# Optimization experiments

Measured on AMD Instinct MI355X. Metric: run time of the kernel, lower is better.

Reference implementation:

```python
import jax, jax.numpy as jnp
import numpy as np

C = 256
EPS = 1e-5


def dwconv3x3(x, w):
    # x: [B,C,H,W], w: [C,1,3,3] depthwise (groups=C)
    return jax.lax.conv_general_dilated(
        x, w, window_strides=(1, 1), padding=((1, 1), (1, 1)),
        dimension_numbers=('NCHW', 'OIHW', 'NCHW'), feature_group_count=x.shape[1])


def bn(x, gamma, beta, mean, var):
    # inference-mode batchnorm over channel dim of NCHW
    inv = gamma * jax.lax.rsqrt(var + EPS)
    return x * inv[:, None, None] + (beta - mean * inv)[:, None, None]


def setup_inputs() -> dict:
    key = jax.random.key(0)
    ks = jax.random.split(key, 8)
    B, H, W = 32, 64, 64
    inp = {
        'x': jax.random.normal(ks[0], (B, C, H, W), jnp.float32),
        'edge_w': jax.random.normal(ks[1], (C, 1, 3, 3), jnp.float32) * 0.1,
        'edge_gamma': jnp.ones((C,), jnp.float32),
        'edge_beta': jnp.zeros((C,), jnp.float32),
        'edge_mean': jnp.zeros((C,), jnp.float32),
        'edge_var': jnp.ones((C,), jnp.float32),
        'fc1_w': jax.random.normal(ks[2], (C // 16, C), jnp.float32) * 0.05,
        'fc2_w': jax.random.normal(ks[3], (C, C // 16), jnp.float32) * 0.05,
        'fusion_w': jax.random.normal(ks[4], (C, 2 * C), jnp.float32) * 0.05,
        'fusion_b': jnp.zeros((C,), jnp.float32),
        'bn1_gamma': jnp.ones((C,), jnp.float32),
        'bn1_beta': jnp.zeros((C,), jnp.float32),
        'bn1_mean': jnp.zeros((C,), jnp.float32),
        'bn1_var': jnp.ones((C,), jnp.float32),
        'deform_w': jax.random.normal(ks[5], (C, 1, 3, 3), jnp.float32) * 0.1,
        'balance_w': jax.random.normal(ks[6], (C, C), jnp.float32) * 0.05,
        'balance_b': jnp.zeros((C,), jnp.float32),
        'bn2_gamma': jnp.ones((C,), jnp.float32),
        'bn2_beta': jnp.zeros((C,), jnp.float32),
        'bn2_mean': jnp.zeros((C,), jnp.float32),
        'bn2_var': jnp.ones((C,), jnp.float32),
    }
    return inp


def reference(x, edge_w, edge_gamma, edge_beta, edge_mean, edge_var,
              fc1_w, fc2_w, fusion_w, fusion_b,
              bn1_gamma, bn1_beta, bn1_mean, bn1_var,
              deform_w, balance_w, balance_b,
              bn2_gamma, bn2_beta, bn2_mean, bn2_var):
    # --- EdgeEnhancementAttention ---
    edge = jax.nn.relu(bn(dwconv3x3(x, edge_w), edge_gamma, edge_beta, edge_mean, edge_var))
    # SE channel attention
    avg = jnp.mean(x, axis=(2, 3))                       # [B,C]
    att = jax.nn.relu(avg @ fc1_w.T)                     # [B,C/16]
    att = jax.nn.sigmoid(att @ fc2_w.T)                  # [B,C]
    enhanced = x * att[:, :, None, None]
    fused = jnp.concatenate([enhanced, edge], axis=1)    # [B,2C,H,W]
    out = jnp.einsum('bchw,oc->bohw', fused, fusion_w) + fusion_b[None, :, None, None]
    out = bn(out, bn1_gamma, bn1_beta, bn1_mean, bn1_var)
    # --- DeformConv2d with zero offsets == plain depthwise 3x3 conv, no bias ---
    out = dwconv3x3(out, deform_w)
    # --- balance: 1x1 conv + BN, then gate by input ---
    out = jnp.einsum('bchw,oc->bohw', out, balance_w) + balance_b[None, :, None, None]
    out = bn(out, bn2_gamma, bn2_beta, bn2_mean, bn2_var)
    return out * x
```

## Files before the change

kernel.cpp:

```cpp
#include <hip/hip_runtime.h>
#include <math.h>

#define HW 4096

typedef unsigned short ushort_t;
typedef short v8s __attribute__((ext_vector_type(8)));
typedef float v4f __attribute__((ext_vector_type(4)));

__device__ __forceinline__ float bf2f(ushort_t u) {
    union { unsigned int i; float f; } v; v.i = ((unsigned int)u) << 16; return v.f;
}
__device__ __forceinline__ ushort_t f2bf(float f) {
    unsigned int x = __float_as_uint(f);
    x += 0x7fffu + ((x >> 16) & 1u);
    return (ushort_t)(x >> 16);
}

__global__ __launch_bounds__(256) void k_consts(
    const float* eg, const float* ebt, const float* em, const float* ev,
    const float* fb,
    const float* g1, const float* b1, const float* m1, const float* v1,
    const float* balb,
    const float* g2, const float* b2, const float* m2, const float* v2,
    float* cbuf)
{
    int c = threadIdx.x;
    float iE = eg[c] * rsqrtf(ev[c] + 1e-5f);
    cbuf[c]       = iE;
    cbuf[256 + c] = ebt[c] - em[c] * iE;
    float i1 = g1[c] * rsqrtf(v1[c] + 1e-5f);
    cbuf[512 + c] = i1;
    cbuf[768 + c] = b1[c] - m1[c] * i1 + fb[c] * i1;
    float i2 = g2[c] * rsqrtf(v2[c] + 1e-5f);
    cbuf[1024 + c] = i2;
    cbuf[1280 + c] = b2[c] - m2[c] * i2 + balb[c] * i2;
}

__global__ __launch_bounds__(256) void k_wcopy(const float* fusw, const float* balw,
                                               ushort_t* fusw2b, ushort_t* balwb)
{
    int o = blockIdx.x, t = threadIdx.x;
    fusw2b[o * 256 + t] = f2bf(fusw[o * 512 + 256 + t]);
    balwb[o * 256 + t]  = f2bf(balw[o * 256 + t]);
}

__global__ __launch_bounds__(256) void k_edge(const float* x, const float* ew,
                                              const float* cbuf, ushort_t* et,
                                              float* avg)
{
    int bid = blockIdx.x;
    int b = bid >> 6;
    int cq = bid & 63;
    int t = threadIdx.x;
    int w = t & 63;
    int pl = t >> 6;
    int c = cq * 4 + pl;
    const float* px = x + ((size_t)(b * 256 + c)) * HW;
    ushort_t* pe = et + ((size_t)(b * 256 + c)) * HW;
    float wt[9];
    #pragma unroll
    for (int k = 0; k < 9; ++k) wt[k] = ew[c * 9 + k];
    float sE = cbuf[c], cE = cbuf[256 + c];
    bool wl = (w > 0), wr = (w < 63);

    float p0l = 0.f, p0c = 0.f, p0r = 0.f;
    float p1l, p1c, p1r;
    p1c = px[w];
    p1l = wl ? px[w - 1] : 0.f;
    p1r = wr ? px[w + 1] : 0.f;
    float s = 0.f;
    #pragma unroll 4
    for (int h = 0; h < 64; ++h) {
        float p2l, p2c, p2r;
        if (h < 63) {
            const float* row = px + (h + 1) * 64;
            p2c = row[w];
            p2l = wl ? row[w - 1] : 0.f;
            p2r = wr ? row[w + 1] : 0.f;
        } else {
            p2l = p2c = p2r = 0.f;
        }
        float a = p0l * wt[0] + p0c * wt[1] + p0r * wt[2]
                + p1l * wt[3] + p1c * wt[4] + p1r * wt[5]
                + p2l * wt[6] + p2c * wt[7] + p2r * wt[8];
        s += p1c;
        float v = a * sE + cE;
        pe[h * 64 + w] = f2bf(v > 0.f ? v : 0.f);
        p0l = p1l; p0c = p1c; p0r = p1r;
        p1l = p2l; p1c = p2c; p1r = p2r;
    }
    #pragma unroll
    for (int off = 32; off > 0; off >>= 1) s += __shfl_down(s, off, 64);
    if ((t & 63) == 0) avg[b * 256 + c] = s * (1.0f / HW);
}

__global__ __launch_bounds__(256) void k_sefold(const float* avg, const float* fc1,
                                                const float* fc2, const float* fusw,
                                                ushort_t* w1b)
{
    int b = blockIdx.x, t = threadIdx.x;
    __shared__ float av[256];
    __shared__ float hid[16];
    av[t] = avg[b * 256 + t];
    __syncthreads();
    if (t < 16) {
        float h = 0.f;
        for (int c = 0; c < 256; ++c) h += av[c] * fc1[t * 256 + c];
        hid[t] = h > 0.f ? h : 0.f;
    }
    __syncthreads();
    float a = 0.f;
    #pragma unroll
    for (int j = 0; j < 16; ++j) a += hid[j] * fc2[t * 16 + j];
    float att = 1.0f / (1.0f + expf(-a));
    ushort_t* wout = w1b + (size_t)b * 65536;
    for (int o = 0; o < 256; ++o)
        wout[o * 256 + t] = f2bf(fusw[o * 512 + t] * att);
}

__global__ __launch_bounds__(256) void k_gemm1(const float* x, const ushort_t* et,
                                               const ushort_t* w1b, const ushort_t* fusw2b,
                                               const float* cbuf, ushort_t* t1)
{
    __shared__ ushort_t At[128 * 64];
    int b = blockIdx.z;
    int hw0 = blockIdx.x * 128;
    int nb = blockIdx.y;
    int t = threadIdx.x;
    int lane = t & 63, wv = t >> 6;
    int quad = lane >> 4, l16 = lane & 15;
    int wr = wv >> 1, wc = wv & 1;

    v4f acc[4][4];
    #pragma unroll
    for (int i = 0; i < 4; ++i)
        #pragma unroll
        for (int j = 0; j < 4; ++j) acc[i][j] = (v4f){0.f, 0.f, 0.f, 0.f};

    int chunk = t & 15;
    int cr0 = t >> 4;

    int oo[4];
    const ushort_t* rowA[4];
    const ushort_t* rowB[4];
    #pragma unroll
    for (int nt = 0; nt < 4; ++nt) {
        int o = nb * 128 + wc * 64 + nt * 16 + l16;
        oo[nt] = o;
        rowA[nt] = w1b + ((size_t)(b * 256 + o)) * 256;
        rowB[nt] = fusw2b + (size_t)o * 256;
    }

    for (int kb = 0; kb < 8; ++kb) {
        __syncthreads();
        #pragma unroll 1
        for (int cr = 0; cr < 4; ++cr) {
            int c_row = cr0 + cr * 16;
            ushort_t e[8];
            if (kb < 4) {
                const float* p = x + ((size_t)b * 256 + (size_t)(kb * 64 + c_row)) * HW
                                 + hw0 + chunk * 8;
                float4 v0 = *(const float4*)p;
                float4 v1 = *(const float4*)(p + 4);
                e[0] = f2bf(v0.x); e[1] = f2bf(v0.y); e[2] = f2bf(v0.z); e[3] = f2bf(v0.w);
                e[4] = f2bf(v1.x); e[5] = f2bf(v1.y); e[6] = f2bf(v1.z); e[7] = f2bf(v1.w);
            } else {
                const ushort_t* p = et + ((size_t)b * 256 + (size_t)((kb - 4) * 64 + c_row)) * HW
                                    + hw0 + chunk * 8;
                uint4 v = *(const uint4*)p;
                unsigned int wd[4] = { v.x, v.y, v.z, v.w };
                #pragma unroll
                for (int i = 0; i < 8; ++i)
                    e[i] = (i & 1) ? (ushort_t)(wd[i >> 1] >> 16) : (ushort_t)(wd[i >> 1] & 0xffff);
            }
            int gb = c_row >> 3, klo = c_row & 7;
            #pragma unroll
            for (int i = 0; i < 8; ++i) {
                int hwl = chunk * 8 + i;
                int g = gb ^ i ^ (chunk & 7);
                At[hwl * 64 + g * 8 + klo] = e[i];
            }
        }
        __syncthreads();
        #pragma unroll
        for (int ks = 0; ks < 64; ks += 32) {
            int kk = ks + quad * 8;
            int kg = kb * 64 + kk;
            v8s bfr[4], afr[4];
            #pragma unroll
            for (int nt = 0; nt < 4; ++nt) {
                const ushort_t* p = (kg < 256) ? (rowA[nt] + kg) : (rowB[nt] + (kg - 256));
                bfr[nt] = *(const v8s*)p;
            }
            #pragma unroll
            for (int mt = 0; mt < 4; ++mt) {
                int ml = wr * 64 + mt * 16 + l16;
                int g = (kk >> 3) ^ (ml & 7) ^ ((ml >> 3) & 7);
                afr[mt] = *(const v8s*)(&At[ml * 64 + g * 8]);
            }
            #pragma unroll
            for (int mt = 0; mt < 4; ++mt)
                #pragma unroll
                for (int nt = 0; nt < 4; ++nt)
                    acc[mt][nt] = __builtin_amdgcn_mfma_f32_16x16x32_bf16(
                        afr[mt], bfr[nt], acc[mt][nt], 0, 0, 0);
        }
    }
    #pragma unroll
    for (int nt = 0; nt < 4; ++nt) {
        int o = oo[nt];
        float s1 = cbuf[512 + o], c1 = cbuf[768 + o];
        #pragma unroll
        for (int mt = 0; mt < 4; ++mt)
            #pragma unroll
            for (int r = 0; r < 4; ++r) {
                int m = hw0 + wr * 64 + mt * 16 + quad * 4 + r;
                t1[((size_t)b * HW + m) * 256 + o] = f2bf(acc[mt][nt][r] * s1 + c1);
            }
    }
}

__global__ __launch_bounds__(256) void k_dw2(const ushort_t* t1, const float* dfw,
                                             ushort_t* t2)
{
    int h = blockIdx.x;
    int b = blockIdx.y;
    int t = threadIdx.x;
    int cg = t & 31;
    int wc = t >> 5;
    int c0 = cg * 8;
    int w0 = wc * 8;

    float acc[8][8];
    #pragma unroll
    for (int w = 0; w < 8; ++w)
        #pragma unroll
        for (int ch = 0; ch < 8; ++ch) acc[w][ch] = 0.f;

    const ushort_t* base = t1 + ((size_t)b * HW) * 256;
    #pragma unroll
    for (int r = 0; r < 3; ++r) {
        int hh = h - 1 + r;
        if (hh < 0 || hh > 63) continue;
        float wtr[3][8];
        #pragma unroll
        for (int d = 0; d < 3; ++d)
            #pragma unroll
            for (int ch = 0; ch < 8; ++ch)
                wtr[d][ch] = dfw[(c0 + ch) * 9 + r * 3 + d];
        const ushort_t* row = base + (size_t)(hh * 64) * 256;
        uint4 rv[10];
        #pragma unroll
        for (int j = 0; j < 10; ++j) {
            int col = w0 - 1 + j;
            if (col >= 0 && col < 64)
                rv[j] = *(const uint4*)(row + (size_t)col * 256 + c0);
            else
                rv[j] = (uint4){0u, 0u, 0u, 0u};
        }
        #pragma unroll
        for (int j = 0; j < 10; ++j) {
            unsigned int wd[4] = { rv[j].x, rv[j].y, rv[j].z, rv[j].w };
            float v[8];
            #pragma unroll
            for (int i = 0; i < 8; ++i)
                v[i] = bf2f((i & 1) ? (ushort_t)(wd[i >> 1] >> 16)
                                    : (ushort_t)(wd[i >> 1] & 0xffff));
            if (j <= 7)
                #pragma unroll
                for (int ch = 0; ch < 8; ++ch) acc[j][ch] += v[ch] * wtr[0][ch];
            if (j >= 1 && j <= 8)
                #pragma unroll
                for (int ch = 0; ch < 8; ++ch) acc[j - 1][ch] += v[ch] * wtr[1][ch];
            if (j >= 2)
                #pragma unroll
                for (int ch = 0; ch < 8; ++ch) acc[j - 2][ch] += v[ch] * wtr[2][ch];
        }
    }
    ushort_t* ob = t2 + ((size_t)b * HW + h * 64 + w0) * 256 + c0;
    #pragma unroll
    for (int w = 0; w < 8; ++w) {
        uint4 ov;
        ov.x = (unsigned int)f2bf(acc[w][0]) | ((unsigned int)f2bf(acc[w][1]) << 16);
        ov.y = (unsigned int)f2bf(acc[w][2]) | ((unsigned int)f2bf(acc[w][3]) << 16);
        ov.z = (unsigned int)f2bf(acc[w][4]) | ((unsigned int)f2bf(acc[w][5]) << 16);
        ov.w = (unsigned int)f2bf(acc[w][6]) | ((unsigned int)f2bf(acc[w][7]) << 16);
        *(uint4*)(ob + (size_t)w * 256) = ov;
    }
}

__global__ __launch_bounds__(256) void k_gemm2(const ushort_t* t2, const ushort_t* balwb,
                                               ushort_t* t3)
{
    __shared__ ushort_t At[128 * 64];
    int b = blockIdx.z;
    int hw0 = blockIdx.x * 128;
    int nb = blockIdx.y;
    int t = threadIdx.x;
    int lane = t & 63, wv = t >> 6;
    int quad = lane >> 4, l16 = lane & 15;
    int wr = wv >> 1, wc = wv & 1;

    v4f acc[4][4];
    #pragma unroll
    for (int i = 0; i < 4; ++i)
        #pragma unroll
        for (int j = 0; j < 4; ++j) acc[i][j] = (v4f){0.f, 0.f, 0.f, 0.f};

    int oo[4];
    const ushort_t* rowW[4];
    #pragma unroll
    for (int nt = 0; nt < 4; ++nt) {
        int o = nb * 128 + wc * 64 + nt * 16 + l16;
        oo[nt] = o;
        rowW[nt] = balwb + (size_t)o * 256;
    }

    for (int kb = 0; kb < 4; ++kb) {
        __syncthreads();
        #pragma unroll
        for (int r2 = 0; r2 < 4; ++r2) {
            int id = r2 * 256 + t;
            int m = id >> 3;
            int kc = (id & 7) * 8;
            uint4 v = *(const uint4*)(t2 + ((size_t)b * HW + hw0 + m) * 256 + kb * 64 + kc);
            int g = (kc >> 3) ^ (m & 7) ^ ((m >> 3) & 7);
            *(uint4*)(&At[m * 64 + g * 8]) = v;
        }
        __syncthreads();
        #pragma unroll
        for (int ks = 0; ks < 64; ks += 32) {
            int kk = ks + quad * 8;
            int kg = kb * 64 + kk;
            v8s bfr[4], afr[4];
            #pragma unroll
            for (int nt = 0; nt < 4; ++nt) bfr[nt] = *(const v8s*)(rowW[nt] + kg);
            #pragma unroll
            for (int mt = 0; mt < 4; ++mt) {
                int ml = wr * 64 + mt * 16 + l16;
                int g = (kk >> 3) ^ (ml & 7) ^ ((ml >> 3) & 7);
                afr[mt] = *(const v8s*)(&At[ml * 64 + g * 8]);
            }
            #pragma unroll
            for (int mt = 0; mt < 4; ++mt)
                #pragma unroll
                for (int nt = 0; nt < 4; ++nt)
                    acc[mt][nt] = __builtin_amdgcn_mfma_f32_16x16x32_bf16(
                        afr[mt], bfr[nt], acc[mt][nt], 0, 0, 0);
        }
    }
    #pragma unroll
    for (int nt = 0; nt < 4; ++nt) {
        int o = oo[nt];
        #pragma unroll
        for (int mt = 0; mt < 4; ++mt)
            #pragma unroll
            for (int r = 0; r < 4; ++r) {
                int m = hw0 + wr * 64 + mt * 16 + quad * 4 + r;
                t3[((size_t)b * HW + m) * 256 + o] = f2bf(acc[mt][nt][r]);
            }
    }
}

__global__ __launch_bounds__(256) void k_final(const ushort_t* t3, const float* x,
                                               const float* cbuf, float* out)
{
    __shared__ float Lt[64 * 65];
    int bid = blockIdx.x;
    int b = bid >> 8;
    int rem = bid & 255;
    int hw0 = (rem >> 2) * 64;
    int c0 = (rem & 3) * 64;
    int t = threadIdx.x;
    #pragma unroll
    for (int r = 0; r < 2; ++r) {
        int idx = r * 256 + t;
        int hwl = idx >> 3;
        int cq = idx & 7;
        uint4 v = *(const uint4*)(t3 + ((size_t)b * HW + hw0 + hwl) * 256 + c0 + cq * 8);
        unsigned int wd[4] = { v.x, v.y, v.z, v.w };
        #pragma unroll
        for (int j = 0; j < 8; ++j) {
            ushort_t u = (j & 1) ? (ushort_t)(wd[j >> 1] >> 16) : (ushort_t)(wd[j >> 1] & 0xffff);
            Lt[(cq * 8 + j) * 65 + hwl] = bf2f(u);
        }
    }
    __syncthreads();
    int hw_l = t & 63;
    int c_l0 = t >> 6;
    #pragma unroll
    for (int j = 0; j < 16; ++j) {
        int c_l = c_l0 * 16 + j;
        int c = c0 + c_l;
        float s2 = cbuf[1024 + c], c2 = cbuf[1280 + c];
        size_t g = ((size_t)b * 256 + c) * HW + hw0 + hw_l;
        float xv = x[g];
        out[g] = (Lt[c_l * 65 + hw_l] * s2 + c2) * xv;
    }
}

extern "C" void kernel_launch(void* const* d_in, const int* in_sizes, int n_in,
                              void* d_out, int out_size, void* d_ws, size_t ws_size,
                              hipStream_t stream)
{
    const float* x    = (const float*)d_in[0];
    const float* ew   = (const float*)d_in[1];
    const float* fc1  = (const float*)d_in[6];
    const float* fc2  = (const float*)d_in[7];
    const float* fusw = (const float*)d_in[8];
    const float* dfw  = (const float*)d_in[14];
    const float* balw = (const float*)d_in[15];
    float* out = (float*)d_out;

    char* ws = (char*)d_ws;
    ushort_t* et     = (ushort_t*)(ws);
    ushort_t* t1     = (ushort_t*)(ws + 67108864);
    ushort_t* t2     = et;
    ushort_t* t3     = t1;
    ushort_t* w1b    = (ushort_t*)(ws + 134217728);
    ushort_t* fusw2b = (ushort_t*)(ws + 138412032);
    ushort_t* balwb  = (ushort_t*)(ws + 138543104);
    float*    avg    = (float*)(ws + 138674176);
    float*    cbuf   = (float*)(ws + 138706944);

    k_consts<<<1, 256, 0, stream>>>((const float*)d_in[2], (const float*)d_in[3],
                                    (const float*)d_in[4], (const float*)d_in[5],
                                    (const float*)d_in[9],
                                    (const float*)d_in[10], (const float*)d_in[11],
                                    (const float*)d_in[12], (const float*)d_in[13],
                                    (const float*)d_in[16],
                                    (const float*)d_in[17], (const float*)d_in[18],
                                    (const float*)d_in[19], (const float*)d_in[20],
                                    cbuf);
    k_wcopy<<<256, 256, 0, stream>>>(fusw, balw, fusw2b, balwb);
    k_edge<<<2048, 256, 0, stream>>>(x, ew, cbuf, et, avg);
    k_sefold<<<32, 256, 0, stream>>>(avg, fc1, fc2, fusw, w1b);
    k_gemm1<<<dim3(32, 2, 32), 256, 0, stream>>>(x, et, w1b, fusw2b, cbuf, t1);
    k_dw2<<<dim3(64, 32), 256, 0, stream>>>(t1, dfw, t2);
    k_gemm2<<<dim3(32, 2, 32), 256, 0, stream>>>(t2, balwb, t3);
    k_final<<<8192, 256, 0, stream>>>(t3, x, cbuf, out);
}
```

Before: 579.2 us.

## Adopt channel-blocked bf16 workspace layout with async LDS double-buffered GEMMs

All intermediates now use one shared workspace in a channel-group-of-8 planar layout. k_edge writes both a bf16 copy of x and the edge output into it, so gemm1 no longer re-reads and converts fp32 x. Both GEMMs now use 512-thread blocks covering all 256 output channels. Their A tiles are staged with global_load_lds into double-buffered shared memory, with B fragments prefetched, so loads overlap MFMA work. k_dw2 and k_final read and write the new layout, which adds a bf16 x copy and heavier block-level LDS use in k_edge.

```diff
diff --git a/kernel.cpp b/kernel.cpp
--- a/kernel.cpp
+++ b/kernel.cpp
@@ -2,6 +2,7 @@
 #include <math.h>
 
 #define HW 4096
+#define PLSTRIDE ((size_t)HW * 8)
 
 typedef unsigned short ushort_t;
 typedef short v8s __attribute__((ext_vector_type(8)));
@@ -14,6 +15,12 @@
     unsigned int x = __float_as_uint(f);
     x += 0x7fffu + ((x >> 16) & 1u);
     return (ushort_t)(x >> 16);
+}
+
+__device__ __forceinline__ void gld16(const ushort_t* g, ushort_t* l) {
+    __builtin_amdgcn_global_load_lds(
+        (__attribute__((address_space(1))) void*)g,
+        (__attribute__((address_space(3))) void*)l, 16, 0, 0);
 }
 
 __global__ __launch_bounds__(256) void k_consts(
@@ -44,50 +51,65 @@
     balwb[o * 256 + t]  = f2bf(balw[o * 256 + t]);
 }
 
-__global__ __launch_bounds__(256) void k_edge(const float* x, const float* ew,
-                                              const float* cbuf, ushort_t* et,
+__global__ __launch_bounds__(512) void k_edge(const float* x, const float* ew,
+                                              const float* cbuf, ushort_t* A,
                                               float* avg)
 {
-    int bid = blockIdx.x;
-    int b = bid >> 6;
-    int cq = bid & 63;
+    __shared__ __align__(16) ushort_t Xs[4096];
+    __shared__ __align__(16) ushort_t Es[4096];
+    int cg = blockIdx.x;
+    int b = blockIdx.y;
     int t = threadIdx.x;
     int w = t & 63;
     int pl = t >> 6;
-    int c = cq * 4 + pl;
+    int c = cg * 8 + pl;
     const float* px = x + ((size_t)(b * 256 + c)) * HW;
-    ushort_t* pe = et + ((size_t)(b * 256 + c)) * HW;
+    ushort_t* AX = A + ((size_t)(b * 64 + cg)) * PLSTRIDE;
+    ushort_t* AE = A + ((size_t)(b * 64 + 32 + cg)) * PLSTRIDE;
     float wt[9];
     #pragma unroll
     for (int k = 0; k < 9; ++k) wt[k] = ew[c * 9 + k];
     float sE = cbuf[c], cE = cbuf[256 + c];
-    bool wl = (w > 0), wr = (w < 63);
+    bool wl = (w > 0), wrr = (w < 63);
 
     float p0l = 0.f, p0c = 0.f, p0r = 0.f;
     float p1l, p1c, p1r;
     p1c = px[w];
     p1l = wl ? px[w - 1] : 0.f;
-    p1r = wr ? px[w + 1] : 0.f;
+    p1r = wrr ? px[w + 1] : 0.f;
     float s = 0.f;
-    #pragma unroll 4
-    for (int h = 0; h < 64; ++h) {
-        float p2l, p2c, p2r;
-        if (h < 63) {
-            const float* row = px + (h + 1) * 64;
-            p2c = row[w];
-            p2l = wl ? row[w - 1] : 0.f;
-            p2r = wr ? row[w + 1] : 0.f;
-        } else {
-            p2l = p2c = p2r = 0.f;
-        }
-        float a = p0l * wt[0] + p0c * wt[1] + p0r * wt[2]
-                + p1l * wt[3] + p1c * wt[4] + p1r * wt[5]
-                + p2l * wt[6] + p2c * wt[7] + p2r * wt[8];
-        s += p1c;
-        float v = a * sE + cE;
-        pe[h * 64 + w] = f2bf(v > 0.f ? v : 0.f);
-        p0l = p1l; p0c = p1c; p0r = p1r;
-        p1l = p2l; p1c = p2c; p1r = p2r;
+    for (int hb = 0; hb < 8; ++hb) {
+        #pragma unroll
+        for (int hi = 0; hi < 8; ++hi) {
+            int h = hb * 8 + hi;
+            float p2l, p2c, p2r;
+            if (h < 63) {
+                const float* row = px + (h + 1) * 64;
+                p2c = row[w];
+                p2l = wl ? row[w - 1] : 0.f;
+                p2r = wrr ? row[w + 1] : 0.f;
+            } else {
+                p2l = p2c = p2r = 0.f;
+            }
+            float a = p0l * wt[0] + p0c * wt[1] + p0r * wt[2]
+                    + p1l * wt[3] + p1c * wt[4] + p1r * wt[5]
+                    + p2l * wt[6] + p2c * wt[7] + p2r * wt[8];
+            s += p1c;
+            float v = a * sE + cE;
+            Es[hi * 512 + w * 8 + pl] = f2bf(v > 0.f ? v : 0.f);
+            Xs[hi * 512 + w * 8 + pl] = f2bf(p1c);
+            p0l = p1l; p0c = p1c; p0r = p1r;
+            p1l = p2l; p1c = p2c; p1r = p2r;
+        }
+        __syncthreads();
+        {
+            int hwg = (hb * 8 + pl) * 64 + w;
+            uint4 vx = *(const uint4*)&Xs[pl * 512 + w * 8];
+            uint4 ve = *(const uint4*)&Es[pl * 512 + w * 8];
+            *(uint4*)(AX + (size_t)hwg * 8) = vx;
+            *(uint4*)(AE + (size_t)hwg * 8) = ve;
+        }
+        __syncthreads();
     }
     #pragma unroll
     for (int off = 32; off > 0; off >>= 1) s += __shfl_down(s, off, 64);
@@ -118,18 +140,17 @@
         wout[o * 256 + t] = f2bf(fusw[o * 512 + t] * att);
 }
 
-__global__ __launch_bounds__(256) void k_gemm1(const float* x, const ushort_t* et,
-                                               const ushort_t* w1b, const ushort_t* fusw2b,
-                                               const float* cbuf, ushort_t* t1)
-{
-    __shared__ ushort_t At[128 * 64];
-    int b = blockIdx.z;
+__global__ __launch_bounds__(512) void k_gemm1(ushort_t* A, const ushort_t* w1b,
+                                               const ushort_t* fusw2b,
+                                               const float* cbuf)
+{
+    __shared__ __align__(16) ushort_t At[2][128 * 64];
     int hw0 = blockIdx.x * 128;
-    int nb = blockIdx.y;
+    int b = blockIdx.y;
     int t = threadIdx.x;
     int lane = t & 63, wv = t >> 6;
     int quad = lane >> 4, l16 = lane & 15;
-    int wr = wv >> 1, wc = wv & 1;
+    int wr = wv >> 2, wc = wv & 3;
 
     v4f acc[4][4];
     #pragma unroll
@@ -137,97 +158,90 @@
         #pragma unroll
         for (int j = 0; j < 4; ++j) acc[i][j] = (v4f){0.f, 0.f, 0.f, 0.f};
 
-    int chunk = t & 15;
-    int cr0 = t >> 4;
-
-    int oo[4];
     const ushort_t* rowA[4];
     const ushort_t* rowB[4];
+    int oo[4];
     #pragma unroll
     for (int nt = 0; nt < 4; ++nt) {
-        int o = nb * 128 + wc * 64 + nt * 16 + l16;
+        int o = wc * 64 + nt * 16 + l16;
         oo[nt] = o;
         rowA[nt] = w1b + ((size_t)(b * 256 + o)) * 256;
         rowB[nt] = fusw2b + (size_t)o * 256;
     }
 
+    int mrow0 = wv * 16 + (lane >> 3);
+    int cswz = (lane & 7) ^ (mrow0 & 7);
+    const ushort_t* srcK = A + ((size_t)(b * 64 + cswz)) * PLSTRIDE
+                             + ((size_t)(hw0 + mrow0)) * 8;
+
+#define STAGE1(bs, kbv) { \
+    const ushort_t* sp = srcK + (size_t)((kbv) * 8) * PLSTRIDE; \
+    gld16(sp, &At[bs][(wv * 16) * 64]); \
+    gld16(sp + 64, &At[bs][(wv * 16 + 8) * 64]); }
+
+#define LDB1(dst, kbv) { \
+    _Pragma("unroll") for (int ks2 = 0; ks2 < 2; ++ks2) { \
+        int kg = (kbv) * 64 + ks2 * 32 + quad * 8; \
+        _Pragma("unroll") for (int nt = 0; nt < 4; ++nt) { \
+            dst[ks2][nt] = ((kbv) < 4) ? *(const v8s*)(rowA[nt] + kg) \
+                                       : *(const v8s*)(rowB[nt] + (kg - 256)); \
+        } } }
+
+#define COMP1(bs, bsrc) { \
+    _Pragma("unroll") for (int ks2 = 0; ks2 < 2; ++ks2) { \
+        v8s afr[4]; \
+        _Pragma("unroll") for (int mt = 0; mt < 4; ++mt) { \
+            int ml = wr * 64 + mt * 16 + l16; \
+            int jj = (ks2 * 4 + quad) ^ (ml & 7); \
+            afr[mt] = *(const v8s*)(&At[bs][ml * 64 + jj * 8]); \
+        } \
+        _Pragma("unroll") for (int mt = 0; mt < 4; ++mt) \
+            _Pragma("unroll") for (int nt = 0; nt < 4; ++nt) \
+                acc[mt][nt] = __builtin_amdgcn_mfma_f32_16x16x32_bf16( \
+                    afr[mt], bsrc[ks2][nt], acc[mt][nt], 0, 0, 0); \
+    } }
+
+    v8s bq0[2][4], bq1[2][4];
+    LDB1(bq0, 0);
+    STAGE1(0, 0);
+    __syncthreads();
+    #pragma unroll
     for (int kb = 0; kb < 8; ++kb) {
+        if ((kb & 1) == 0) {
+            if (kb < 7) { STAGE1(1, kb + 1); LDB1(bq1, kb + 1); }
+            COMP1(0, bq0);
+        } else {
+            if (kb < 7) { STAGE1(0, kb + 1); LDB1(bq0, kb + 1); }
+            COMP1(1, bq1);
+        }
         __syncthreads();
-        #pragma unroll 1
-        for (int cr = 0; cr < 4; ++cr) {
-            int c_row = cr0 + cr * 16;
-            ushort_t e[8];
-            if (kb < 4) {
-                const float* p = x + ((size_t)b * 256 + (size_t)(kb * 64 + c_row)) * HW
-                                 + hw0 + chunk * 8;
-                float4 v0 = *(const float4*)p;
-                float4 v1 = *(const float4*)(p + 4);
-                e[0] = f2bf(v0.x); e[1] = f2bf(v0.y); e[2] = f2bf(v0.z); e[3] = f2bf(v0.w);
-                e[4] = f2bf(v1.x); e[5] = f2bf(v1.y); e[6] = f2bf(v1.z); e[7] = f2bf(v1.w);
-            } else {
-                const ushort_t* p = et + ((size_t)b * 256 + (size_t)((kb - 4) * 64 + c_row)) * HW
-                                    + hw0 + chunk * 8;
-                uint4 v = *(const uint4*)p;
-                unsigned int wd[4] = { v.x, v.y, v.z, v.w };
-                #pragma unroll
-                for (int i = 0; i < 8; ++i)
-                    e[i] = (i & 1) ? (ushort_t)(wd[i >> 1] >> 16) : (ushort_t)(wd[i >> 1] & 0xffff);
-            }
-            int gb = c_row >> 3, klo = c_row & 7;
-            #pragma unroll
-            for (int i = 0; i < 8; ++i) {
-                int hwl = chunk * 8 + i;
-                int g = gb ^ i ^ (chunk & 7);
-                At[hwl * 64 + g * 8 + klo] = e[i];
-            }
-        }
-        __syncthreads();
-        #pragma unroll
-        for (int ks = 0; ks < 64; ks += 32) {
-            int kk = ks + quad * 8;
-            int kg = kb * 64 + kk;
-            v8s bfr[4], afr[4];
-            #pragma unroll
-            for (int nt = 0; nt < 4; ++nt) {
-                const ushort_t* p = (kg < 256) ? (rowA[nt] + kg) : (rowB[nt] + (kg - 256));
-                bfr[nt] = *(const v8s*)p;
-            }
-            #pragma unroll
-            for (int mt = 0; mt < 4; ++mt) {
-                int ml = wr * 64 + mt * 16 + l16;
-                int g = (kk >> 3) ^ (ml & 7) ^ ((ml >> 3) & 7);
-                afr[mt] = *(const v8s*)(&At[ml * 64 + g * 8]);
-            }
-            #pragma unroll
-            for (int mt = 0; mt < 4; ++mt)
-                #pragma unroll
-                for (int nt = 0; nt < 4; ++nt)
-                    acc[mt][nt] = __builtin_amdgcn_mfma_f32_16x16x32_bf16(
-                        afr[mt], bfr[nt], acc[mt][nt], 0, 0, 0);
-        }
-    }
+    }
+#undef STAGE1
+#undef LDB1
+#undef COMP1
+
     #pragma unroll
     for (int nt = 0; nt < 4; ++nt) {
         int o = oo[nt];
         float s1 = cbuf[512 + o], c1 = cbuf[768 + o];
+        ushort_t* op = A + ((size_t)(b * 64 + 32 + (o >> 3))) * PLSTRIDE + (o & 7);
         #pragma unroll
         for (int mt = 0; mt < 4; ++mt)
             #pragma unroll
             for (int r = 0; r < 4; ++r) {
                 int m = hw0 + wr * 64 + mt * 16 + quad * 4 + r;
-                t1[((size_t)b * HW + m) * 256 + o] = f2bf(acc[mt][nt][r] * s1 + c1);
+                op[(size_t)m * 8] = f2bf(acc[mt][nt][r] * s1 + c1);
             }
     }
 }
 
-__global__ __launch_bounds__(256) void k_dw2(const ushort_t* t1, const float* dfw,
-                                             ushort_t* t2)
+__global__ __launch_bounds__(256) void k_dw2(ushort_t* A, const float* dfw)
 {
     int h = blockIdx.x;
     int b = blockIdx.y;
     int t = threadIdx.x;
-    int cg = t & 31;
-    int wc = t >> 5;
+    int wc = t & 7;
+    int cg = t >> 3;
     int c0 = cg * 8;
     int w0 = wc * 8;
 
@@ -237,7 +251,7 @@
         #pragma unroll
         for (int ch = 0; ch < 8; ++ch) acc[w][ch] = 0.f;
 
-    const ushort_t* base = t1 + ((size_t)b * HW) * 256;
+    const ushort_t* pE = A + ((size_t)(b * 64 + 32 + cg)) * PLSTRIDE;
     #pragma unroll
     for (int r = 0; r < 3; ++r) {
         int hh = h - 1 + r;
@@ -248,13 +262,13 @@
             #pragma unroll
             for (int ch = 0; ch < 8; ++ch)
                 wtr[d][ch] = dfw[(c0 + ch) * 9 + r * 3 + d];
-        const ushort_t* row = base + (size_t)(hh * 64) * 256;
+        const ushort_t* row = pE + (size_t)(hh * 64) * 8;
         uint4 rv[10];
         #pragma unroll
         for (int j = 0; j < 10; ++j) {
             int col = w0 - 1 + j;
             if (col >= 0 && col < 64)
-                rv[j] = *(const uint4*)(row + (size_t)col * 256 + c0);
+                rv[j] = *(const uint4*)(row + (size_t)col * 8);
             else
                 rv[j] = (uint4){0u, 0u, 0u, 0u};
         }
@@ -277,7 +291,7 @@
                 for (int ch = 0; ch < 8; ++ch) acc[j - 2][ch] += v[ch] * wtr[2][ch];
         }
     }
-    ushort_t* ob = t2 + ((size_t)b * HW + h * 64 + w0) * 256 + c0;
+    ushort_t* pX = A + ((size_t)(b * 64 + cg)) * PLSTRIDE + (size_t)(h * 64 + w0) * 8;
     #pragma unroll
     for (int w = 0; w < 8; ++w) {
         uint4 ov;
@@ -285,21 +299,19 @@
         ov.y = (unsigned int)f2bf(acc[w][2]) | ((unsigned int)f2bf(acc[w][3]) << 16);
         ov.z = (unsigned int)f2bf(acc[w][4]) | ((unsigned int)f2bf(acc[w][5]) << 16);
         ov.w = (unsigned int)f2bf(acc[w][6]) | ((unsigned int)f2bf(acc[w][7]) << 16);
-        *(uint4*)(ob + (size_t)w * 256) = ov;
-    }
-}
-
-__global__ __launch_bounds__(256) void k_gemm2(const ushort_t* t2, const ushort_t* balwb,
-                                               ushort_t* t3)
-{
-    __shared__ ushort_t At[128 * 64];
-    int b = blockIdx.z;
+        *(uint4*)(pX + (size_t)w * 8) = ov;
+    }
+}
+
+__global__ __launch_bounds__(512) void k_gemm2(ushort_t* A, const ushort_t* balwb)
+{
+    __shared__ __align__(16) ushort_t At[2][128 * 64];
     int hw0 = blockIdx.x * 128;
-    int nb = blockIdx.y;
+    int b = blockIdx.y;
     int t = threadIdx.x;
     int lane = t & 63, wv = t >> 6;
     int quad = lane >> 4, l16 = lane & 15;
-    int wr = wv >> 1, wc = wv & 1;
+    int wr = wv >> 2, wc = wv & 3;
 
     v4f acc[4][4];
     #pragma unroll
@@ -307,62 +319,80 @@
         #pragma unroll
         for (int j = 0; j < 4; ++j) acc[i][j] = (v4f){0.f, 0.f, 0.f, 0.f};
 
+    const ushort_t* rowW[4];
     int oo[4];
-    const ushort_t* rowW[4];
     #pragma unroll
     for (int nt = 0; nt < 4; ++nt) {
-        int o = nb * 128 + wc * 64 + nt * 16 + l16;
+        int o = wc * 64 + nt * 16 + l16;
         oo[nt] = o;
         rowW[nt] = balwb + (size_t)o * 256;
     }
 
+    int mrow0 = wv * 16 + (lane >> 3);
+    int cswz = (lane & 7) ^ (mrow0 & 7);
+    const ushort_t* srcK = A + ((size_t)(b * 64 + cswz)) * PLSTRIDE
+                             + ((size_t)(hw0 + mrow0)) * 8;
+
+#define STAGE2(bs, kbv) { \
+    const ushort_t* sp = srcK + (size_t)((kbv) * 8) * PLSTRIDE; \
+    gld16(sp, &At[bs][(wv * 16) * 64]); \
+    gld16(sp + 64, &At[bs][(wv * 16 + 8) * 64]); }
+
+#define LDB2(dst, kbv) { \
+    _Pragma("unroll") for (int ks2 = 0; ks2 < 2; ++ks2) { \
+        int kg = (kbv) * 64 + ks2 * 32 + quad * 8; \
+        _Pragma("unroll") for (int nt = 0; nt < 4; ++nt) \
+            dst[ks2][nt] = *(const v8s*)(rowW[nt] + kg); \
+    } }
+
+#define COMP2(bs, bsrc) { \
+    _Pragma("unroll") for (int ks2 = 0; ks2 < 2; ++ks2) { \
+        v8s afr[4]; \
+        _Pragma("unroll") for (int mt = 0; mt < 4; ++mt) { \
+            int ml = wr * 64 + mt * 16 + l16; \
+            int jj = (ks2 * 4 + quad) ^ (ml & 7); \
+            afr[mt] = *(const v8s*)(&At[bs][ml * 64 + jj * 8]); \
+        } \
+        _Pragma("unroll") for (int mt = 0; mt < 4; ++mt) \
+            _Pragma("unroll") for (int nt = 0; nt < 4; ++nt) \
+                acc[mt][nt] = __builtin_amdgcn_mfma_f32_16x16x32_bf16( \
+                    afr[mt], bsrc[ks2][nt], acc[mt][nt], 0, 0, 0); \
+    } }
+
+    v8s bq0[2][4], bq1[2][4];
+    LDB2(bq0, 0);
+    STAGE2(0, 0);
+    __syncthreads();
+    #pragma unroll
     for (int kb = 0; kb < 4; ++kb) {
+        if ((kb & 1) == 0) {
+            if (kb < 3) { STAGE2(1, kb + 1); LDB2(bq1, kb + 1); }
+            COMP2(0, bq0);
+        } else {
+            if (kb < 3) { STAGE2(0, kb + 1); LDB2(bq0, kb + 1); }
+            COMP2(1, bq1);
+        }
         __syncthreads();
-        #pragma unroll
-        for (int r2 = 0; r2 < 4; ++r2) {
-            int id = r2 * 256 + t;
-            int m = id >> 3;
-            int kc = (id & 7) * 8;
-            uint4 v = *(const uint4*)(t2 + ((size_t)b * HW + hw0 + m) * 256 + kb * 64 + kc);
-            int g = (kc >> 3) ^ (m & 7) ^ ((m >> 3) & 7);
-            *(uint4*)(&At[m * 64 + g * 8]) = v;
-        }
-        __syncthreads();
-        #pragma unroll
-        for (int ks = 0; ks < 64; ks += 32) {
-            int kk = ks + quad * 8;
-            int kg = kb * 64 + kk;
-            v8s bfr[4], afr[4];
-            #pragma unroll
-            for (int nt = 0; nt < 4; ++nt) bfr[nt] = *(const v8s*)(rowW[nt] + kg);
-            #pragma unroll
-            for (int mt = 0; mt < 4; ++mt) {
-                int ml = wr * 64 + mt * 16 + l16;
-                int g = (kk >> 3) ^ (ml & 7) ^ ((ml >> 3) & 7);
-                afr[mt] = *(const v8s*)(&At[ml * 64 + g * 8]);
-            }
-            #pragma unroll
-            for (int mt = 0; mt < 4; ++mt)
-                #pragma unroll
-                for (int nt = 0; nt < 4; ++nt)
-                    acc[mt][nt] = __builtin_amdgcn_mfma_f32_16x16x32_bf16(
-                        afr[mt], bfr[nt], acc[mt][nt], 0, 0, 0);
-        }
-    }
+    }
+#undef STAGE2
+#undef LDB2
+#undef COMP2
+
     #pragma unroll
     for (int nt = 0; nt < 4; ++nt) {
         int o = oo[nt];
+        ushort_t* op = A + ((size_t)(b * 64 + 32 + (o >> 3))) * PLSTRIDE + (o & 7);
         #pragma unroll
         for (int mt = 0; mt < 4; ++mt)
             #pragma unroll
             for (int r = 0; r < 4; ++r) {
                 int m = hw0 + wr * 64 + mt * 16 + quad * 4 + r;
-                t3[((size_t)b * HW + m) * 256 + o] = f2bf(acc[mt][nt][r]);
+                op[(size_t)m * 8] = f2bf(acc[mt][nt][r]);
             }
     }
 }
 
-__global__ __launch_bounds__(256) void k_final(const ushort_t* t3, const float* x,
+__global__ __launch_bounds__(256) void k_final(const ushort_t* A, const float* x,
                                                const float* cbuf, float* out)
 {
     __shared__ float Lt[64 * 65];
@@ -377,7 +407,8 @@
         int idx = r * 256 + t;
         int hwl = idx >> 3;
         int cq = idx & 7;
-        uint4 v = *(const uint4*)(t3 + ((size_t)b * HW + hw0 + hwl) * 256 + c0 + cq * 8);
+        uint4 v = *(const uint4*)(A + ((size_t)(b * 64 + 32 + (c0 >> 3) + cq)) * PLSTRIDE
+                                    + (size_t)(hw0 + hwl) * 8);
         unsigned int wd[4] = { v.x, v.y, v.z, v.w };
         #pragma unroll
         for (int j = 0; j < 8; ++j) {
@@ -413,10 +444,7 @@
     float* out = (float*)d_out;
 
     char* ws = (char*)d_ws;
-    ushort_t* et     = (ushort_t*)(ws);
-    ushort_t* t1     = (ushort_t*)(ws + 67108864);
-    ushort_t* t2     = et;
-    ushort_t* t3     = t1;
+    ushort_t* A      = (ushort_t*)(ws);
     ushort_t* w1b    = (ushort_t*)(ws + 134217728);
     ushort_t* fusw2b = (ushort_t*)(ws + 138412032);
     ushort_t* balwb  = (ushort_t*)(ws + 138543104);
@@ -433,10 +461,10 @@
                                     (const float*)d_in[19], (const float*)d_in[20],
                                     cbuf);
     k_wcopy<<<256, 256, 0, stream>>>(fusw, balw, fusw2b, balwb);
-    k_edge<<<2048, 256, 0, stream>>>(x, ew, cbuf, et, avg);
+    k_edge<<<dim3(32, 32), 512, 0, stream>>>(x, ew, cbuf, A, avg);
     k_sefold<<<32, 256, 0, stream>>>(avg, fc1, fc2, fusw, w1b);
-    k_gemm1<<<dim3(32, 2, 32), 256, 0, stream>>>(x, et, w1b, fusw2b, cbuf, t1);
-    k_dw2<<<dim3(64, 32), 256, 0, stream>>>(t1, dfw, t2);
-    k_gemm2<<<dim3(32, 2, 32), 256, 0, stream>>>(t2, balwb, t3);
-    k_final<<<8192, 256, 0, stream>>>(t3, x, cbuf, out);
-}
+    k_gemm1<<<dim3(32, 32), 512, 0, stream>>>(A, w1b, fusw2b, cbuf);
+    k_dw2<<<dim3(64, 32), 256, 0, stream>>>(A, dfw);
+    k_gemm2<<<dim3(32, 32), 512, 0, stream>>>(A, balwb);
+    k_final<<<8192, 256, 0, stream>>>(A, x, cbuf, out);
+}
```

Measured after the change: 609.2 us. 5.2% more time.
